# Optimization experiments

Hardware: AMD Instinct MI355X
Metric: run time of the kernel (lower is better)

The kernel has to match this reference:

```python
import jax, jax.numpy as jnp
import numpy as np

B, S, E, H, DK, DV, V, FH = 2, 1024, 1024, 16, 64, 64, 32000, 512


def _posenc(seq_len, d_model, n=10000.0):
    pos = jnp.arange(seq_len, dtype=jnp.float32)[:, None]            # [S,1]
    i2 = jnp.arange(0, d_model, 2, dtype=jnp.float32)                 # [E/2]
    ang = pos / jnp.power(n, i2 / d_model)                            # [S,E/2]
    return jnp.stack([jnp.sin(ang), jnp.cos(ang)], axis=-1).reshape(seq_len, d_model)


def _norm(x, g, b, eps=1e-15):
    m = jnp.mean(x, axis=-1, keepdims=True)
    v = jnp.var(x, axis=-1, keepdims=True)  # unbiased=False
    return g * (x - m) * jax.lax.rsqrt(v + eps) + b


def _ff(x, w1, b1, w2, b2):
    return jax.nn.relu(x @ w1 + b1) @ w2 + b2


def _mha(xq, xkv, wqkv, bqkv, wo, bo, causal):
    # wqkv: [3,H,E,d], bqkv: [3,H,d]  (stacked per-head linears)
    q = jnp.einsum('bse,hek->bhsk', xq, wqkv[0]) + bqkv[0][None, :, None, :]
    k = jnp.einsum('bse,hek->bhsk', xkv, wqkv[1]) + bqkv[1][None, :, None, :]
    v = jnp.einsum('bse,hev->bhsv', xkv, wqkv[2]) + bqkv[2][None, :, None, :]
    s = jnp.einsum('bhqk,bhsk->bhqs', q, k) / jnp.sqrt(jnp.float32(DK))
    if causal:
        mask = jnp.triu(jnp.ones((S, S), dtype=bool), 1)
        s = jnp.where(mask[None, None], -jnp.inf, s)
    p = jax.nn.softmax(s, axis=-1)
    o = jnp.einsum('bhqs,bhsv->bhqv', p, v)
    o = o.transpose(0, 2, 1, 3).reshape(xq.shape[0], S, H * DV)
    return o @ wo + bo


def setup_inputs():
    key = jax.random.key(0)
    ks = iter(jax.random.split(key, 40))

    def rn(shape, scale=0.02):
        return jax.random.normal(next(ks), shape, dtype=jnp.float32) * scale

    inp = {
        'src': jax.random.randint(next(ks), (B, S), 0, V, dtype=jnp.int32),
        'trg': jax.random.randint(next(ks), (B, S), 0, V, dtype=jnp.int32),
        'emb_enc': rn((V, E), 1.0),
        'emb_dec': rn((V, E), 1.0),
        'qkv_e': rn((3, H, E, DK)), 'bqkv_e': rn((3, H, DK)),
        'wo_e': rn((H * DV, E)), 'bo_e': rn((E,)),
        'qkv_m': rn((3, H, E, DK)), 'bqkv_m': rn((3, H, DK)),
        'wo_m': rn((H * DV, E)), 'bo_m': rn((E,)),
        'qkv_c': rn((3, H, E, DK)), 'bqkv_c': rn((3, H, DK)),
        'wo_c': rn((H * DV, E)), 'bo_c': rn((E,)),
        'gamma': jnp.ones((5, E), jnp.float32),
        'beta': jnp.zeros((5, E), jnp.float32),
        'ff_w1': rn((2, E, FH)), 'ff_b1': rn((2, FH)),
        'ff_w2': rn((2, FH, E)), 'ff_b2': rn((2, E)),
        'w_out': rn((E, V)), 'b_out': rn((V,)),
    }
    return inp


def reference(src, trg, emb_enc, emb_dec, qkv_e, bqkv_e, wo_e, bo_e,
              qkv_m, bqkv_m, wo_m, bo_m, qkv_c, bqkv_c, wo_c, bo_c,
              gamma, beta, ff_w1, ff_b1, ff_w2, ff_b2, w_out, b_out):
    pe = _posenc(S, E)
    # ---- encoder ----
    x = emb_enc[src] + pe
    a = _mha(x, x, qkv_e, bqkv_e, wo_e, bo_e, causal=False)
    n1 = _norm(x + a, gamma[0], beta[0])
    f = _ff(n1, ff_w1[0], ff_b1[0], ff_w2[0], ff_b2[0])
    enc = _norm(n1 + f, gamma[1], beta[1])
    # ---- decoder ----
    y = emb_dec[trg] + pe
    a = _mha(y, y, qkv_m, bqkv_m, wo_m, bo_m, causal=True)
    n1d = _norm(y + a, gamma[2], beta[2])
    a2 = _mha(n1d, enc, qkv_c, bqkv_c, wo_c, bo_c, causal=False)
    n2d = _norm(n1d + a2, gamma[3], beta[3])
    f = _ff(n2d, ff_w1[1], ff_b1[1], ff_w2[1], ff_b2[1])
    n3d = _norm(n2d + f, gamma[4], beta[4])
    logits = n3d @ w_out + b_out
    return jax.nn.softmax(logits, axis=-1)
```

## Files before the change

kernel.cpp:

```cpp
#include <hip/hip_runtime.h>
#include <hip/hip_bf16.h>
#include <hip/hip_fp16.h>
#include <math.h>

namespace {

constexpr int kB = 2, kS = 1024, kE = 1024, kH = 16, kD = 64, kV = 32000, kFH = 512;
constexpr int kBS = kB * kS;
constexpr int kHD = kH * kD;

typedef __attribute__((ext_vector_type(8))) short bf16x8;
typedef __attribute__((ext_vector_type(8))) unsigned short u16x8;
typedef __attribute__((ext_vector_type(4))) float f32x4;

#define GLDS(g, l) __builtin_amdgcn_global_load_lds(                          \
      (const __attribute__((address_space(1))) void*)(g),                     \
      (__attribute__((address_space(3))) void*)(l), 16, 0, 0)

struct TSeg {
  const float* src;
  __hip_bfloat16* dst;
  int R, C, bpi, off;
};
struct TcastArgs { TSeg s[11]; };

__global__ __launch_bounds__(256) void prep_k(
    const int* __restrict__ src, const int* __restrict__ trg,
    const float* __restrict__ emb_e, const float* __restrict__ emb_d,
    float* __restrict__ enc_x, __hip_bfloat16* __restrict__ enc_xb,
    float* __restrict__ dec_x, __hip_bfloat16* __restrict__ dec_xb,
    TcastArgs a) {
  int bid = blockIdx.x;
  if (bid < 2 * kBS) {
    int which = bid >> 11;
    int row = bid & (kBS - 1);
    const int* tok = which ? trg : src;
    const float* emb = which ? emb_d : emb_e;
    float* out = which ? dec_x : enc_x;
    __hip_bfloat16* outb = which ? dec_xb : enc_xb;
    int s = row & (kS - 1);
    int t = tok[row];
    const float4* sv4 = (const float4*)(emb + (size_t)t * kE);
    int e4 = threadIdx.x;
    float4 aa = sv4[e4];
    const float kLn = 0.017988946039015984f;
    int p0 = e4 * 2, p1 = p0 + 1;
    float a0 = (float)s * __expf(-(float)p0 * kLn);
    float a1 = (float)s * __expf(-(float)p1 * kLn);
    float4 v = make_float4(aa.x + sinf(a0), aa.y + cosf(a0),
                           aa.z + sinf(a1), aa.w + cosf(a1));
    ((float4*)(out + (size_t)row * kE))[e4] = v;
    union { __hip_bfloat16 h[4]; short4 s4; } u;
    u.h[0] = __float2bfloat16(v.x); u.h[1] = __float2bfloat16(v.y);
    u.h[2] = __float2bfloat16(v.z); u.h[3] = __float2bfloat16(v.w);
    ((short4*)(outb + (size_t)row * kE))[e4] = u.s4;
    return;
  }
  bid -= 2 * kBS;
  __shared__ float tile[32][33];
  int si = 0;
#pragma unroll
  for (int i = 1; i < 11; ++i) si = (bid >= a.s[i].off) ? i : si;
  const TSeg sg = a.s[si];
  int local = bid - sg.off;
  int item = local / sg.bpi;
  int rem  = local % sg.bpi;
  int nbx = sg.C >> 5;
  int c0 = (rem % nbx) * 32, r0 = (rem / nbx) * 32;
  const float* srcp = sg.src + (size_t)item * sg.R * sg.C;
  __hip_bfloat16* dstp = sg.dst + (size_t)item * sg.R * sg.C;
  int tx = threadIdx.x & 31, ty = threadIdx.x >> 5;
#pragma unroll
  for (int i = 0; i < 32; i += 8)
    tile[ty + i][tx] = srcp[(size_t)(r0 + ty + i) * sg.C + c0 + tx];
  __syncthreads();
#pragma unroll
  for (int i = 0; i < 32; i += 8)
    dstp[(size_t)(c0 + ty + i) * sg.R + r0 + tx] = __float2bfloat16(tile[tx][ty + i]);
}

__global__ __launch_bounds__(256) void vtrans_k(const __hip_bfloat16* __restrict__ v,
                                                int sV, __hip_bfloat16* __restrict__ vt) {
  __shared__ unsigned short tile[32][34];
  int s0 = blockIdx.x * 32, d0 = blockIdx.y * 32, bh = blockIdx.z;
  int b = bh >> 4, h = bh & 15;
  int tx = threadIdx.x & 31, ty = threadIdx.x >> 5;
  const unsigned short* src = (const unsigned short*)v;
  unsigned short* dst = (unsigned short*)vt;
#pragma unroll
  for (int i = 0; i < 32; i += 8)
    tile[ty + i][tx] = src[(size_t)(b * kS + s0 + ty + i) * sV + h * 64 + d0 + tx];
  __syncthreads();
#pragma unroll
  for (int i = 0; i < 32; i += 8)
    dst[(size_t)(bh * 64 + d0 + ty + i) * kS + s0 + tx] = tile[tx][ty + i];
}

__global__ __launch_bounds__(256) void gemm_bf16_k(
    const __hip_bfloat16* __restrict__ A,
    const __hip_bfloat16* __restrict__ Bt,
    const float* __restrict__ bias,
    void* __restrict__ Cout,
    int N, int K, int mode, int gridM) {
  __shared__ __align__(16) char L[3][16384];
  const int nwg = gridDim.x, id = blockIdx.x;
  const int swz = (id & 7) * (nwg >> 3) + (id >> 3);
  const int bm = (swz % gridM) * 128, bn = (swz / gridM) * 128;
  const int tid = threadIdx.x, w = tid >> 6, lane = tid & 63;
  const int wr = w >> 1, wc = w & 1;
  const int lr = lane & 15, kg = lane >> 4;
  const int NT = K >> 5;
  const __hip_bfloat16* Ag = A + (size_t)bm * K;
  const __hip_bfloat16* Bg = Bt + (size_t)bn * K;

  auto stage = [&](int t) {
    const int buf = t % 3, k0 = t * 32;
#pragma unroll
    for (int j = 0; j < 2; ++j) {
      int slot = w * 64 + lane + j * 256;
      int row = slot >> 2;
      int cs = (slot & 3) ^ ((row >> 1) & 3);
      GLDS(Ag + (size_t)row * K + k0 + cs * 8, L[buf] + w * 1024 + j * 4096);
      GLDS(Bg + (size_t)row * K + k0 + cs * 8, L[buf] + 8192 + w * 1024 + j * 4096);
    }
  };

  f32x4 acc[4][4] = {};
  stage(0);
  stage(1);
  asm volatile("s_waitcnt vmcnt(4)" ::: "memory");
  __builtin_amdgcn_s_barrier();

  for (int t = 0; t < NT; ++t) {
    const char* buf = L[t % 3];
    if (t + 2 < NT) stage(t + 2);
    bf16x8 af[4], bfr[4];
#pragma unroll
    for (int i = 0; i < 4; ++i) {
      int row = wr * 64 + i * 16 + lr;
      af[i] = *(const bf16x8*)(buf + row * 64 + ((kg ^ ((row >> 1) & 3)) << 4));
    }
#pragma unroll
    for (int j = 0; j < 4; ++j) {
      int row = wc * 64 + j * 16 + lr;
      bfr[j] = *(const bf16x8*)(buf + 8192 + row * 64 + ((kg ^ ((row >> 1) & 3)) << 4));
    }
    __builtin_amdgcn_s_setprio(1);
#pragma unroll
    for (int i = 0; i < 4; ++i)
#pragma unroll
      for (int j = 0; j < 4; ++j)
        acc[i][j] = __builtin_amdgcn_mfma_f32_16x16x32_bf16(af[i], bfr[j], acc[i][j], 0, 0, 0);
    __builtin_amdgcn_s_setprio(0);
    if (t + 2 < NT)
      asm volatile("s_waitcnt vmcnt(4) lgkmcnt(0)" ::: "memory");
    else
      asm volatile("s_waitcnt vmcnt(0) lgkmcnt(0)" ::: "memory");
    __builtin_amdgcn_s_barrier();
  }

  float* Cf = (float*)Cout;
  __hip_bfloat16* Cb = (__hip_bfloat16*)Cout;
#pragma unroll
  for (int j = 0; j < 4; ++j) {
    int col = bn + wc * 64 + j * 16 + lr;
    float bc = bias[col];
#pragma unroll
    for (int i = 0; i < 4; ++i) {
      int rbase = bm + wr * 64 + i * 16 + kg * 4;
#pragma unroll
      for (int r = 0; r < 4; ++r) {
        float val = acc[i][j][r] + bc;
        if (mode & 1) val = fmaxf(val, 0.0f);
        if (mode < 2) Cf[(size_t)(rbase + r) * N + col] = val;
        else          Cb[(size_t)(rbase + r) * N + col] = __float2bfloat16(val);
      }
    }
  }
}

__global__ __launch_bounds__(256) void gemm64_k(
    const __hip_bfloat16* __restrict__ A,
    const __hip_bfloat16* __restrict__ Bt,
    const float* __restrict__ bias,
    void* __restrict__ Cout,
    int N, int K, int mode, int gridM) {
  __shared__ __align__(16) char L[3][8192];
  const int nwg = gridDim.x, id = blockIdx.x;
  const int swz = (id & 7) * (nwg >> 3) + (id >> 3);
  const int bm = (swz % gridM) * 64, bn = (swz / gridM) * 64;
  const int tid = threadIdx.x, w = tid >> 6, lane = tid & 63;
  const int wr = w >> 1, wc = w & 1;
  const int lr = lane & 15, kg = lane >> 4;
  const int NT = K >> 5;
  const __hip_bfloat16* Ag = A + (size_t)bm * K;
  const __hip_bfloat16* Bg = Bt + (size_t)bn * K;

  auto stage = [&](int t) {
    const int buf = t % 3, k0 = t * 32;
    int row = tid >> 2;
    int cs = (tid & 3) ^ ((row >> 1) & 3);
    GLDS(Ag + (size_t)row * K + k0 + cs * 8, L[buf] + tid * 16);
    GLDS(Bg + (size_t)row * K + k0 + cs * 8, L[buf] + 4096 + tid * 16);
  };

  f32x4 acc[2][2] = {};
  stage(0);
  stage(1);
  asm volatile("s_waitcnt vmcnt(2)" ::: "memory");
  __builtin_amdgcn_s_barrier();

  for (int t = 0; t < NT; ++t) {
    const char* buf = L[t % 3];
    if (t + 2 < NT) stage(t + 2);
    bf16x8 af[2], bfr[2];
#pragma unroll
    for (int i = 0; i < 2; ++i) {
      int row = wr * 32 + i * 16 + lr;
      af[i] = *(const bf16x8*)(buf + row * 64 + ((kg ^ ((row >> 1) & 3)) << 4));
    }
#pragma unroll
    for (int j = 0; j < 2; ++j) {
      int row = wc * 32 + j * 16 + lr;
      bfr[j] = *(const bf16x8*)(buf + 4096 + row * 64 + ((kg ^ ((row >> 1) & 3)) << 4));
    }
    __builtin_amdgcn_s_setprio(1);
#pragma unroll
    for (int i = 0; i < 2; ++i)
#pragma unroll
      for (int j = 0; j < 2; ++j)
        acc[i][j] = __builtin_amdgcn_mfma_f32_16x16x32_bf16(af[i], bfr[j], acc[i][j], 0, 0, 0);
    __builtin_amdgcn_s_setprio(0);
    if (t + 2 < NT)
      asm volatile("s_waitcnt vmcnt(2) lgkmcnt(0)" ::: "memory");
    else
      asm volatile("s_waitcnt vmcnt(0) lgkmcnt(0)" ::: "memory");
    __builtin_amdgcn_s_barrier();
  }

  float* Cf = (float*)Cout;
  __hip_bfloat16* Cb = (__hip_bfloat16*)Cout;
#pragma unroll
  for (int j = 0; j < 2; ++j) {
    int col = bn + wc * 32 + j * 16 + lr;
    float bc = bias[col];
#pragma unroll
    for (int i = 0; i < 2; ++i) {
      int rbase = bm + wr * 32 + i * 16 + kg * 4;
#pragma unroll
      for (int r = 0; r < 4; ++r) {
        float val = acc[i][j][r] + bc;
        if (mode & 1) val = fmaxf(val, 0.0f);
        if (mode < 2) Cf[(size_t)(rbase + r) * N + col] = val;
        else          Cb[(size_t)(rbase + r) * N + col] = __float2bfloat16(val);
      }
    }
  }
}

__global__ __launch_bounds__(512, 2) void gemm256_k(
    const __hip_bfloat16* __restrict__ A,
    const __hip_bfloat16* __restrict__ Bt,
    const float* __restrict__ bias,
    __half* __restrict__ C,
    int N, int K, int gridM) {
  __shared__ __align__(16) char L[3][32768];
  const int tid = threadIdx.x, w = tid >> 6, lane = tid & 63;
  const int wm = w >> 2, wn = w & 3;
  const int lr = lane & 15, kg = lane >> 4;
  const int nwg = gridDim.x, id = blockIdx.x;
  const int swz = (id & 7) * (nwg >> 3) + (id >> 3);
  const int bm = (swz % gridM) * 256, bn = (swz / gridM) * 256;
  const int NT = K >> 5;
  const __hip_bfloat16* Ag = A + (size_t)bm * K;
  const __hip_bfloat16* Bg = Bt + (size_t)bn * K;

  auto stage = [&](int t) {
    const int buf = t % 3, k0 = t * 32;
#pragma unroll
    for (int j = 0; j < 2; ++j) {
      int slot = w * 64 + lane + j * 512;
      int row = slot >> 2;
      int cs = (slot & 3) ^ ((row >> 1) & 3);
      GLDS(Ag + (size_t)row * K + k0 + cs * 8, L[buf] + w * 1024 + j * 8192);
      GLDS(Bg + (size_t)row * K + k0 + cs * 8, L[buf] + 16384 + w * 1024 + j * 8192);
    }
  };

  f32x4 acc[8][4] = {};
  stage(0);
  stage(1);
  asm volatile("s_waitcnt vmcnt(4)" ::: "memory");
  __builtin_amdgcn_s_barrier();

  for (int t = 0; t < NT; ++t) {
    const char* buf = L[t % 3];
    if (t + 2 < NT) stage(t + 2);
    bf16x8 af[8], bfr[4];
#pragma unroll
    for (int mg = 0; mg < 8; ++mg) {
      int row = wm * 128 + mg * 16 + lr;
      af[mg] = *(const bf16x8*)(buf + row * 64 + ((kg ^ ((row >> 1) & 3)) << 4));
    }
#pragma unroll
    for (int n = 0; n < 4; ++n) {
      int row = wn * 64 + n * 16 + lr;
      bfr[n] = *(const bf16x8*)(buf + 16384 + row * 64 + ((kg ^ ((row >> 1) & 3)) << 4));
    }
    __builtin_amdgcn_s_setprio(1);
#pragma unroll
    for (int mg = 0; mg < 8; ++mg)
#pragma unroll
      for (int n = 0; n < 4; ++n)
        acc[mg][n] = __builtin_amdgcn_mfma_f32_16x16x32_bf16(af[mg], bfr[n], acc[mg][n], 0, 0, 0);
    __builtin_amdgcn_s_setprio(0);
    if (t + 2 < NT)
      asm volatile("s_waitcnt vmcnt(4) lgkmcnt(0)" ::: "memory");
    else
      asm volatile("s_waitcnt vmcnt(0) lgkmcnt(0)" ::: "memory");
    __builtin_amdgcn_s_barrier();
  }

#pragma unroll
  for (int mg = 0; mg < 8; ++mg) {
    int rbase = bm + wm * 128 + mg * 16 + (kg << 2);
#pragma unroll
    for (int n = 0; n < 4; ++n) {
      int col = bn + (wn << 6) + n * 16 + lr;
      float bc = bias[col];
#pragma unroll
      for (int r = 0; r < 4; ++r)
        C[(size_t)(rbase + r) * N + col] = __float2half(acc[mg][n][r] + bc);
    }
  }
}

__global__ __launch_bounds__(256) void attn_mfma_k(
    const __hip_bfloat16* __restrict__ q, int sQ,
    const __hip_bfloat16* __restrict__ k, int sK,
    const __hip_bfloat16* __restrict__ vt,
    __hip_bfloat16* __restrict__ o,
    int causal) {
  __shared__ __align__(16) char Ks[3][8192];
  __shared__ __align__(16) char Vs[3][8192];
  __shared__ __align__(16) char Ps[4][2304];
  const int tid = threadIdx.x, w = tid >> 6, l = tid & 63;
  const int lr = l & 15, lg = l >> 4;
  const int q0 = blockIdx.x * 64, h = blockIdx.y, b = blockIdx.z;

  const int qrow = q0 + w * 16 + lr;
  const __hip_bfloat16* qp = q + (size_t)(b * kS + qrow) * sQ + h * 64 + lg * 8;
  bf16x8 aQ0 = *(const bf16x8*)qp;
  bf16x8 aQ1 = *(const bf16x8*)(qp + 32);

  f32x4 oacc[4] = {};
  float mrun[4], lrun[4];
#pragma unroll
  for (int r = 0; r < 4; ++r) { mrun[r] = -INFINITY; lrun[r] = 0.0f; }

  const int ntiles = causal ? ((q0 >> 6) + 1) : (kS >> 6);
  const int diagT = causal ? (q0 >> 6) : -1;
  const char* kbase = (const char*)(k + (size_t)(b * kS) * sK + h * 64);
  const char* vbase = (const char*)(vt + (size_t)((b * kH + h) * 64) * kS);
  char* Pw = Ps[w];

  auto stage = [&](int t) {
    const int buf = t % 3, kv0 = t * 64;
#pragma unroll
    for (int i = 0; i < 2; ++i) {
      int slot = w * 128 + i * 64 + l;
      int row = slot >> 3, sl = slot & 7, c = sl ^ (row & 7);
      GLDS(kbase + (size_t)(kv0 + row) * sK * 2 + c * 16, Ks[buf] + (w * 128 + i * 64) * 16);
      GLDS(vbase + (size_t)row * kS * 2 + kv0 * 2 + c * 16, Vs[buf] + (w * 128 + i * 64) * 16);
    }
  };

  stage(0);
  if (ntiles > 1) {
    stage(1);
    asm volatile("s_waitcnt vmcnt(4)" ::: "memory");
  } else {
    asm volatile("s_waitcnt vmcnt(0)" ::: "memory");
  }
  __builtin_amdgcn_s_barrier();

  for (int t = 0; t < ntiles; ++t) {
    const int kv0 = t * 64;
    const char* Kb = Ks[t % 3];
    const char* Vb = Vs[t % 3];
    if (t + 2 < ntiles) stage(t + 2);

    f32x4 sacc[4] = {};
#pragma unroll
    for (int nf = 0; nf < 4; ++nf) {
      int key = nf * 16 + lr;
#pragma unroll
      for (int kf = 0; kf < 2; ++kf) {
        int ch = (lg + kf * 4) ^ (key & 7);
        bf16x8 bK = *(const bf16x8*)(Kb + key * 128 + ch * 16);
        sacc[nf] = __builtin_amdgcn_mfma_f32_16x16x32_bf16(kf ? aQ1 : aQ0, bK, sacc[nf], 0, 0, 0);
      }
    }

#pragma unroll
    for (int r = 0; r < 4; ++r) {
      int row16 = lg * 4 + r;
      int qg = q0 + w * 16 + row16;
      float sv[4];
#pragma unroll
      for (int nf = 0; nf < 4; ++nf) {
        float s = sacc[nf][r] * 0.125f;
        if (t == diagT && (kv0 + nf * 16 + lr) > qg) s = -INFINITY;
        sv[nf] = s;
      }
      float mx = fmaxf(fmaxf(sv[0], sv[1]), fmaxf(sv[2], sv[3]));
#pragma unroll
      for (int m = 1; m < 16; m <<= 1) mx = fmaxf(mx, __shfl_xor(mx, m));
      if (mx > mrun[r] + 8.0f) {
        float sc = __expf(mrun[r] - mx);
        mrun[r] = mx;
        lrun[r] *= sc;
#pragma unroll
        for (int nfd = 0; nfd < 4; ++nfd) oacc[nfd][r] *= sc;
      }
      float base = mrun[r];
      float rs = 0.0f;
#pragma unroll
      for (int nf = 0; nf < 4; ++nf) {
        float p = __expf(sv[nf] - base);
        rs += p;
        *(__hip_bfloat16*)(Pw + row16 * 144 + (nf * 16 + lr) * 2) = __float2bfloat16(p);
      }
#pragma unroll
      for (int m = 1; m < 16; m <<= 1) rs += __shfl_xor(rs, m);
      lrun[r] += rs;
    }

    bf16x8 aP0 = *(const bf16x8*)(Pw + lr * 144 + (lg * 8) * 2);
    bf16x8 aP1 = *(const bf16x8*)(Pw + lr * 144 + (lg * 8 + 32) * 2);
#pragma unroll
    for (int nfd = 0; nfd < 4; ++nfd) {
      int d = nfd * 16 + lr;
#pragma unroll
      for (int kf = 0; kf < 2; ++kf) {
        int ch = (lg + kf * 4) ^ (d & 7);
        bf16x8 bV = *(const bf16x8*)(Vb + d * 128 + ch * 16);
        oacc[nfd] = __builtin_amdgcn_mfma_f32_16x16x32_bf16(kf ? aP1 : aP0, bV, oacc[nfd], 0, 0, 0);
      }
    }

    if (t + 1 < ntiles) {
      if (t + 2 < ntiles)
        asm volatile("s_waitcnt vmcnt(4) lgkmcnt(0)" ::: "memory");
      else
        asm volatile("s_waitcnt vmcnt(0) lgkmcnt(0)" ::: "memory");
      __builtin_amdgcn_s_barrier();
    }
  }

#pragma unroll
  for (int r = 0; r < 4; ++r) {
    float inv = 1.0f / lrun[r];
    int rowg = q0 + w * 16 + lg * 4 + r;
#pragma unroll
    for (int nfd = 0; nfd < 4; ++nfd)
      o[(size_t)(b * kS + rowg) * kHD + h * 64 + nfd * 16 + lr] =
          __float2bfloat16(oacc[nfd][r] * inv);
  }
}

__global__ __launch_bounds__(256) void ln_res_k(const float* __restrict__ a,
                                                const float* __restrict__ b,
                                                const float* __restrict__ gamma,
                                                const float* __restrict__ beta,
                                                float* __restrict__ out,
                                                __hip_bfloat16* __restrict__ outb) {
  __shared__ float sh[10];
  int row = blockIdx.x, tid = threadIdx.x;
  const float4* a4 = (const float4*)(a + (size_t)row * kE);
  const float4* b4 = (const float4*)(b + (size_t)row * kE);
  float4 t = a4[tid], u = b4[tid];
  t.x += u.x; t.y += u.y; t.z += u.z; t.w += u.w;
  float s = t.x + t.y + t.z + t.w;
  float q2 = t.x * t.x + t.y * t.y + t.z * t.z + t.w * t.w;
  for (int o = 32; o > 0; o >>= 1) { s += __shfl_down(s, o); q2 += __shfl_down(q2, o); }
  int lane = tid & 63, wid = tid >> 6;
  if (lane == 0) { sh[wid] = s; sh[4 + wid] = q2; }
  __syncthreads();
  if (tid == 0) {
    float S2 = sh[0] + sh[1] + sh[2] + sh[3];
    float Q2 = sh[4] + sh[5] + sh[6] + sh[7];
    float mean = S2 * (1.0f / kE);
    float var = Q2 * (1.0f / kE) - mean * mean;
    sh[8] = mean;
    sh[9] = rsqrtf(var + 1e-15f);
  }
  __syncthreads();
  float mean = sh[8], inv = sh[9];
  float4 g = ((const float4*)gamma)[tid], be = ((const float4*)beta)[tid];
  float4 v;
  v.x = g.x * ((t.x - mean) * inv) + be.x;
  v.y = g.y * ((t.y - mean) * inv) + be.y;
  v.z = g.z * ((t.z - mean) * inv) + be.z;
  v.w = g.w * ((t.w - mean) * inv) + be.w;
  ((float4*)(out + (size_t)row * kE))[tid] = v;
  union { __hip_bfloat16 h[4]; short4 s4; } uo;
  uo.h[0] = __float2bfloat16(v.x); uo.h[1] = __float2bfloat16(v.y);
  uo.h[2] = __float2bfloat16(v.z); uo.h[3] = __float2bfloat16(v.w);
  ((short4*)(outb + (size_t)row * kE))[tid] = uo.s4;
}

__global__ __launch_bounds__(512) void softmax_rows_k(const __half* __restrict__ lgt,
                                                      float* __restrict__ out) {
  __shared__ float sh[18];
  int row = blockIdx.x;
  const u16x8* x8 = (const u16x8*)(lgt + (size_t)row * kV);
  const int n8 = kV / 8;
  int tid = threadIdx.x;
  u16x8 v[8];
  float m = -INFINITY, sum = 0.0f;
#pragma unroll
  for (int i = 0; i < 8; ++i) {
    int idx = tid + i * 512;
    if (idx < n8) {
      v[i] = x8[idx];
      union { u16x8 u; __half h[8]; } cv; cv.u = v[i];
      float f[8];
#pragma unroll
      for (int j = 0; j < 8; ++j) f[j] = __half2float(cv.h[j]);
      float mx = f[0];
#pragma unroll
      for (int j = 1; j < 8; ++j) mx = fmaxf(mx, f[j]);
      float nm = fmaxf(m, mx);
      float add = 0.0f;
#pragma unroll
      for (int j = 0; j < 8; ++j) add += __expf(f[j] - nm);
      sum = sum * __expf(m - nm) + add;
      m = nm;
    }
  }
  for (int o = 32; o > 0; o >>= 1) {
    float om = __shfl_down(m, o), os = __shfl_down(sum, o);
    float nm = fmaxf(m, om);
    sum = sum * __expf(m - nm) + os * __expf(om - nm);
    m = nm;
  }
  int lane = tid & 63, wid = tid >> 6;
  if (lane == 0) { sh[wid] = m; sh[8 + wid] = sum; }
  __syncthreads();
  if (tid == 0) {
    float M = sh[0], S2 = 0.0f;
#pragma unroll
    for (int i2 = 1; i2 < 8; ++i2) M = fmaxf(M, sh[i2]);
#pragma unroll
    for (int i2 = 0; i2 < 8; ++i2) S2 += sh[8 + i2] * __expf(sh[i2] - M);
    sh[16] = M;
    sh[17] = 1.0f / S2;
  }
  __syncthreads();
  float M = sh[16], rcp = sh[17];
#pragma unroll
  for (int i = 0; i < 8; ++i) {
    int idx = tid + i * 512;
    if (idx < n8) {
      union { u16x8 u; __half h[8]; } cv; cv.u = v[i];
      float4 o0, o1;
      o0.x = __expf(__half2float(cv.h[0]) - M) * rcp;
      o0.y = __expf(__half2float(cv.h[1]) - M) * rcp;
      o0.z = __expf(__half2float(cv.h[2]) - M) * rcp;
      o0.w = __expf(__half2float(cv.h[3]) - M) * rcp;
      o1.x = __expf(__half2float(cv.h[4]) - M) * rcp;
      o1.y = __expf(__half2float(cv.h[5]) - M) * rcp;
      o1.z = __expf(__half2float(cv.h[6]) - M) * rcp;
      o1.w = __expf(__half2float(cv.h[7]) - M) * rcp;
      float* dst = out + (size_t)row * kV + idx * 8;
      ((float4*)dst)[0] = o0;
      ((float4*)dst)[1] = o1;
    }
  }
}

}

extern "C" void kernel_launch(void* const* d_in, const int* in_sizes, int n_in,
                              void* d_out, int out_size, void* d_ws, size_t ws_size,
                              hipStream_t stream) {
  const int*   src    = (const int*)d_in[0];
  const int*   trg    = (const int*)d_in[1];
  const float* emb_e  = (const float*)d_in[2];
  const float* emb_d  = (const float*)d_in[3];
  const float* qkv_e  = (const float*)d_in[4];
  const float* bqkv_e = (const float*)d_in[5];
  const float* wo_e   = (const float*)d_in[6];
  const float* bo_e   = (const float*)d_in[7];
  const float* qkv_m  = (const float*)d_in[8];
  const float* bqkv_m = (const float*)d_in[9];
  const float* wo_m   = (const float*)d_in[10];
  const float* bo_m   = (const float*)d_in[11];
  const float* qkv_c  = (const float*)d_in[12];
  const float* bqkv_c = (const float*)d_in[13];
  const float* wo_c   = (const float*)d_in[14];
  const float* bo_c   = (const float*)d_in[15];
  const float* gamma  = (const float*)d_in[16];
  const float* beta   = (const float*)d_in[17];
  const float* ffw1   = (const float*)d_in[18];
  const float* ffb1   = (const float*)d_in[19];
  const float* ffw2   = (const float*)d_in[20];
  const float* ffb2   = (const float*)d_in[21];
  const float* wout   = (const float*)d_in[22];
  const float* bout   = (const float*)d_in[23];
  float* out = (float*)d_out;

  char* base = (char*)d_ws;
  const size_t R = (size_t)kBS * kE;
  const size_t WE = (size_t)kHD * kE;
  float* enc_x = (float*)base;
  float* dec_x = enc_x + R;
  float* t1    = dec_x + R;
  float* n1    = t1 + R;
  float* n_enc = n1 + R;
  __hip_bfloat16* bb     = (__hip_bfloat16*)(n_enc + R);
  __hip_bfloat16* enc_xb = bb;
  __hip_bfloat16* n1b    = enc_xb + R;
  __hip_bfloat16* n_encb = n1b + R;
  __hip_bfloat16* qkvb   = n_encb + R;
  __hip_bfloat16* kvb    = qkvb + 3 * R;
  __hip_bfloat16* qb1    = kvb + 2 * R;
  __hip_bfloat16* vtb    = qb1 + R;
  __hip_bfloat16* ao16   = vtb + R;
  __hip_bfloat16* ffhb   = ao16 + R;
  __hip_bfloat16* Wqkv_e = ffhb + R / 2;
  __hip_bfloat16* Wqkv_m = Wqkv_e + 3 * WE;
  __hip_bfloat16* Wqkv_c = Wqkv_m + 3 * WE;
  __hip_bfloat16* Wo_e   = Wqkv_c + 3 * WE;
  __hip_bfloat16* Wo_m   = Wo_e + WE;
  __hip_bfloat16* Wo_c   = Wo_m + WE;
  __hip_bfloat16* Wf1a   = Wo_c + WE;
  __hip_bfloat16* Wf1b   = Wf1a + (size_t)kE * kFH;
  __hip_bfloat16* Wf2a   = Wf1b + (size_t)kE * kFH;
  __hip_bfloat16* Wf2b   = Wf2a + (size_t)kFH * kE;
  const size_t lgtBytes = (size_t)kBS * kV * sizeof(__half);
  __hip_bfloat16* dec_xb = (__hip_bfloat16*)(base + lgtBytes);
  __hip_bfloat16* Wv     = dec_xb + R;
  __half* lgt = (__half*)base;

  auto gemmb = [&](const __hip_bfloat16* A, const __hip_bfloat16* Bt, const float* bias,
                   void* C, int M, int N, int K, int mode) {
    int gridM = M / 128;
    gemm_bf16_k<<<dim3(gridM * (N / 128)), 256, 0, stream>>>(A, Bt, bias, C, N, K, mode, gridM);
  };
  auto gemmb64 = [&](const __hip_bfloat16* A, const __hip_bfloat16* Bt, const float* bias,
                     void* C, int M, int N, int K, int mode) {
    int gridM = M / 64;
    gemm64_k<<<dim3(gridM * (N / 64)), 256, 0, stream>>>(A, Bt, bias, C, N, K, mode, gridM);
  };
  auto vtrans = [&](const __hip_bfloat16* v, int sV) {
    vtrans_k<<<dim3(kS / 32, kD / 32, kB * kH), 256, 0, stream>>>(v, sV, vtb);
  };
  auto attn = [&](const __hip_bfloat16* q, int sQ, const __hip_bfloat16* k, int sK,
                  int causal) {
    attn_mfma_k<<<dim3(kS / 64, kH, kB), 256, 0, stream>>>(q, sQ, k, sK, vtb, ao16, causal);
  };
  auto ln = [&](const float* a, const float* b2, int sel, float* o1, __hip_bfloat16* o2) {
    ln_res_k<<<kBS, 256, 0, stream>>>(a, b2, gamma + sel * kE, beta + sel * kE, o1, o2);
  };

  {
    TcastArgs a;
    const size_t EF = (size_t)kE * kFH;
    a.s[0]  = {qkv_e,       Wqkv_e, kE, kD,   64,    0};
    a.s[1]  = {qkv_m,       Wqkv_m, kE, kD,   64,    3072};
    a.s[2]  = {qkv_c,       Wqkv_c, kE, kD,   64,    6144};
    a.s[3]  = {wo_e,        Wo_e,   kHD, kE,  1024,  9216};
    a.s[4]  = {wo_m,        Wo_m,   kHD, kE,  1024,  10240};
    a.s[5]  = {wo_c,        Wo_c,   kHD, kE,  1024,  11264};
    a.s[6]  = {ffw1,        Wf1a,   kE, kFH,  512,   12288};
    a.s[7]  = {ffw1 + EF,   Wf1b,   kE, kFH,  512,   12800};
    a.s[8]  = {ffw2,        Wf2a,   kFH, kE,  512,   13312};
    a.s[9]  = {ffw2 + EF,   Wf2b,   kFH, kE,  512,   13824};
    a.s[10] = {wout,        Wv,     kE, kV,   32000, 14336};
    prep_k<<<2 * kBS + 46336, 256, 0, stream>>>(src, trg, emb_e, emb_d,
                                                enc_x, enc_xb, dec_x, dec_xb, a);
  }

  gemmb(enc_xb, Wqkv_e, bqkv_e, qkvb, kBS, 3 * kHD, kE, 2);
  vtrans(qkvb + 2 * kHD, 3 * kHD);
  attn(qkvb, 3 * kHD, qkvb + kHD, 3 * kHD, 0);
  gemmb64(ao16, Wo_e, bo_e, t1, kBS, kE, kHD, 0);
  ln(enc_x, t1, 0, n1, n1b);
  gemmb64(n1b, Wf1a, ffb1, ffhb, kBS, kFH, kE, 3);
  gemmb64(ffhb, Wf2a, ffb2, t1, kBS, kE, kFH, 0);
  ln(n1, t1, 1, n_enc, n_encb);

  gemmb(dec_xb, Wqkv_m, bqkv_m, qkvb, kBS, 3 * kHD, kE, 2);
  vtrans(qkvb + 2 * kHD, 3 * kHD);
  attn(qkvb, 3 * kHD, qkvb + kHD, 3 * kHD, 1);
  gemmb64(ao16, Wo_m, bo_m, t1, kBS, kE, kHD, 0);
  ln(dec_x, t1, 2, n1, n1b);

  gemmb64(n1b, Wqkv_c, bqkv_c, qb1, kBS, kHD, kE, 2);
  gemmb64(n_encb, Wqkv_c + WE, bqkv_c + kHD, kvb, kBS, 2 * kHD, kE, 2);
  vtrans(kvb + kHD, 2 * kHD);
  attn(qb1, kHD, kvb, 2 * kHD, 0);
  gemmb64(ao16, Wo_c, bo_c, t1, kBS, kE, kHD, 0);
  ln(n1, t1, 3, enc_x, enc_xb);

  gemmb64(enc_xb, Wf1b, ffb1 + kFH, ffhb, kBS, kFH, kE, 3);
  gemmb64(ffhb, Wf2b, ffb2 + kE, t1, kBS, kE, kFH, 0);
  ln(enc_x, t1, 4, dec_x, dec_xb);

  gemm256_k<<<dim3((kBS / 256) * (kV / 256)), 512, 0, stream>>>(
      dec_xb, Wv, bout, lgt, kV, kE, kBS / 256);
  softmax_rows_k<<<kBS, 512, 0, stream>>>(lgt, out);
}
```

Before: 611.7 us.

## Batch independent encoder and decoder self-attention stages into dual-launch kernels

Encoder and decoder self-attention chains are independent, so the QKV GEMM, V transpose, attention, output projection and layernorm for both now run as single launches that pick their operands from the grid index. This doubles the work per launch, aiming to fill the GPU better and cut launch overhead and tail effects. The workspace is re-laid out at fixed MiB offsets with aliased buffers, and the unused fp32 layernorm outputs are skipped. The aliasing carries a risk of overlapping live buffers.

```diff
diff --git a/kernel.cpp b/kernel.cpp
--- a/kernel.cpp
+++ b/kernel.cpp
@@ -8,6 +8,7 @@
 constexpr int kB = 2, kS = 1024, kE = 1024, kH = 16, kD = 64, kV = 32000, kFH = 512;
 constexpr int kBS = kB * kS;
 constexpr int kHD = kH * kD;
+constexpr size_t kMiB = 1u << 20;
 
 typedef __attribute__((ext_vector_type(8))) short bf16x8;
 typedef __attribute__((ext_vector_type(8))) unsigned short u16x8;
@@ -79,10 +80,9 @@
     dstp[(size_t)(c0 + ty + i) * sg.R + r0 + tx] = __float2bfloat16(tile[tx][ty + i]);
 }
 
-__global__ __launch_bounds__(256) void vtrans_k(const __hip_bfloat16* __restrict__ v,
-                                                int sV, __hip_bfloat16* __restrict__ vt) {
+__device__ __forceinline__ void vtrans_body(const __hip_bfloat16* v, int sV,
+                                            __hip_bfloat16* vt, int s0, int d0, int bh) {
   __shared__ unsigned short tile[32][34];
-  int s0 = blockIdx.x * 32, d0 = blockIdx.y * 32, bh = blockIdx.z;
   int b = bh >> 4, h = bh & 15;
   int tx = threadIdx.x & 31, ty = threadIdx.x >> 5;
   const unsigned short* src = (const unsigned short*)v;
@@ -96,14 +96,24 @@
     dst[(size_t)(bh * 64 + d0 + ty + i) * kS + s0 + tx] = tile[tx][ty + i];
 }
 
-__global__ __launch_bounds__(256) void gemm_bf16_k(
-    const __hip_bfloat16* __restrict__ A,
-    const __hip_bfloat16* __restrict__ Bt,
-    const float* __restrict__ bias,
-    void* __restrict__ Cout,
-    int N, int K, int mode, int gridM) {
+__global__ __launch_bounds__(256) void vtrans_k(const __hip_bfloat16* __restrict__ v,
+                                                int sV, __hip_bfloat16* __restrict__ vt) {
+  vtrans_body(v, sV, vt, blockIdx.x * 32, blockIdx.y * 32, blockIdx.z);
+}
+
+__global__ __launch_bounds__(256) void vtrans_dual_k(
+    const __hip_bfloat16* __restrict__ v0, __hip_bfloat16* __restrict__ vt0,
+    const __hip_bfloat16* __restrict__ v1, __hip_bfloat16* __restrict__ vt1, int sV) {
+  int z = blockIdx.z;
+  int which = z >> 5, bh = z & 31;
+  vtrans_body(which ? v1 : v0, sV, which ? vt1 : vt0,
+              blockIdx.x * 32, blockIdx.y * 32, bh);
+}
+
+__device__ __forceinline__ void gemm128_body(
+    const __hip_bfloat16* A, const __hip_bfloat16* Bt, const float* bias, void* Cout,
+    int N, int K, int mode, int gridM, int id, int nwg) {
   __shared__ __align__(16) char L[3][16384];
-  const int nwg = gridDim.x, id = blockIdx.x;
   const int swz = (id & 7) * (nwg >> 3) + (id >> 3);
   const int bm = (swz % gridM) * 128, bn = (swz / gridM) * 128;
   const int tid = threadIdx.x, w = tid >> 6, lane = tid & 63;
@@ -179,14 +189,25 @@
   }
 }
 
-__global__ __launch_bounds__(256) void gemm64_k(
-    const __hip_bfloat16* __restrict__ A,
-    const __hip_bfloat16* __restrict__ Bt,
-    const float* __restrict__ bias,
-    void* __restrict__ Cout,
+struct G2 { const __hip_bfloat16* A; const __hip_bfloat16* Bt; const float* bias; void* C; };
+
+__global__ __launch_bounds__(256) void gemm_bf16_k(
+    const __hip_bfloat16* __restrict__ A, const __hip_bfloat16* __restrict__ Bt,
+    const float* __restrict__ bias, void* __restrict__ Cout,
     int N, int K, int mode, int gridM) {
+  gemm128_body(A, Bt, bias, Cout, N, K, mode, gridM, blockIdx.x, gridDim.x);
+}
+
+__global__ __launch_bounds__(256) void gemm_dual_k(G2 g0, G2 g1, int N, int K,
+                                                   int mode, int gridM) {
+  const G2& g = blockIdx.y ? g1 : g0;
+  gemm128_body(g.A, g.Bt, g.bias, g.C, N, K, mode, gridM, blockIdx.x, gridDim.x);
+}
+
+__device__ __forceinline__ void gemm64_body(
+    const __hip_bfloat16* A, const __hip_bfloat16* Bt, const float* bias, void* Cout,
+    int N, int K, int mode, int gridM, int id, int nwg) {
   __shared__ __align__(16) char L[3][8192];
-  const int nwg = gridDim.x, id = blockIdx.x;
   const int swz = (id & 7) * (nwg >> 3) + (id >> 3);
   const int bm = (swz % gridM) * 64, bn = (swz / gridM) * 64;
   const int tid = threadIdx.x, w = tid >> 6, lane = tid & 63;
@@ -258,11 +279,22 @@
   }
 }
 
+__global__ __launch_bounds__(256) void gemm64_k(
+    const __hip_bfloat16* __restrict__ A, const __hip_bfloat16* __restrict__ Bt,
+    const float* __restrict__ bias, void* __restrict__ Cout,
+    int N, int K, int mode, int gridM) {
+  gemm64_body(A, Bt, bias, Cout, N, K, mode, gridM, blockIdx.x, gridDim.x);
+}
+
+__global__ __launch_bounds__(256) void gemm64_dual_k(G2 g0, G2 g1, int N, int K,
+                                                     int mode, int gridM) {
+  const G2& g = blockIdx.y ? g1 : g0;
+  gemm64_body(g.A, g.Bt, g.bias, g.C, N, K, mode, gridM, blockIdx.x, gridDim.x);
+}
+
 __global__ __launch_bounds__(512, 2) void gemm256_k(
-    const __hip_bfloat16* __restrict__ A,
-    const __hip_bfloat16* __restrict__ Bt,
-    const float* __restrict__ bias,
-    __half* __restrict__ C,
+    const __hip_bfloat16* __restrict__ A, const __hip_bfloat16* __restrict__ Bt,
+    const float* __restrict__ bias, __half* __restrict__ C,
     int N, int K, int gridM) {
   __shared__ __align__(16) char L[3][32768];
   const int tid = threadIdx.x, w = tid >> 6, lane = tid & 63;
@@ -335,18 +367,15 @@
   }
 }
 
-__global__ __launch_bounds__(256) void attn_mfma_k(
-    const __hip_bfloat16* __restrict__ q, int sQ,
-    const __hip_bfloat16* __restrict__ k, int sK,
-    const __hip_bfloat16* __restrict__ vt,
-    __hip_bfloat16* __restrict__ o,
-    int causal) {
+__device__ __forceinline__ void attn_body(
+    const __hip_bfloat16* q, int sQ, const __hip_bfloat16* k, int sK,
+    const __hip_bfloat16* vt, __hip_bfloat16* o, int causal, int qblk, int h, int b) {
   __shared__ __align__(16) char Ks[3][8192];
   __shared__ __align__(16) char Vs[3][8192];
   __shared__ __align__(16) char Ps[4][2304];
   const int tid = threadIdx.x, w = tid >> 6, l = tid & 63;
   const int lr = l & 15, lg = l >> 4;
-  const int q0 = blockIdx.x * 64, h = blockIdx.y, b = blockIdx.z;
+  const int q0 = qblk * 64;
 
   const int qrow = q0 + w * 16 + lr;
   const __hip_bfloat16* qp = q + (size_t)(b * kS + qrow) * sQ + h * 64 + lg * 8;
@@ -358,8 +387,8 @@
 #pragma unroll
   for (int r = 0; r < 4; ++r) { mrun[r] = -INFINITY; lrun[r] = 0.0f; }
 
-  const int ntiles = causal ? ((q0 >> 6) + 1) : (kS >> 6);
-  const int diagT = causal ? (q0 >> 6) : -1;
+  const int ntiles = causal ? (qblk + 1) : (kS >> 6);
+  const int diagT = causal ? qblk : -1;
   const char* kbase = (const char*)(k + (size_t)(b * kS) * sK + h * 64);
   const char* vbase = (const char*)(vt + (size_t)((b * kH + h) * 64) * kS);
   char* Pw = Ps[w];
@@ -469,14 +498,29 @@
   }
 }
 
-__global__ __launch_bounds__(256) void ln_res_k(const float* __restrict__ a,
-                                                const float* __restrict__ b,
-                                                const float* __restrict__ gamma,
-                                                const float* __restrict__ beta,
-                                                float* __restrict__ out,
-                                                __hip_bfloat16* __restrict__ outb) {
+__global__ __launch_bounds__(256) void attn_mfma_k(
+    const __hip_bfloat16* __restrict__ q, int sQ,
+    const __hip_bfloat16* __restrict__ k, int sK,
+    const __hip_bfloat16* __restrict__ vt,
+    __hip_bfloat16* __restrict__ o, int causal) {
+  attn_body(q, sQ, k, sK, vt, o, causal, blockIdx.x, blockIdx.y, blockIdx.z);
+}
+
+struct A2 { const __hip_bfloat16* q; const __hip_bfloat16* k;
+            const __hip_bfloat16* vt; __hip_bfloat16* o; int causal; };
+
+__global__ __launch_bounds__(256) void attn_dual_k(A2 a0, A2 a1, int sQ, int sK) {
+  int z = blockIdx.z;
+  int which = z >> 1, b = z & 1;
+  const A2& a = which ? a1 : a0;
+  attn_body(a.q, sQ, a.k, sK, a.vt, a.o, a.causal, blockIdx.x, blockIdx.y, b);
+}
+
+__device__ __forceinline__ void ln_body(const float* a, const float* b,
+                                        const float* gamma, const float* beta,
+                                        float* out, __hip_bfloat16* outb, int row) {
   __shared__ float sh[10];
-  int row = blockIdx.x, tid = threadIdx.x;
+  int tid = threadIdx.x;
   const float4* a4 = (const float4*)(a + (size_t)row * kE);
   const float4* b4 = (const float4*)(b + (size_t)row * kE);
   float4 t = a4[tid], u = b4[tid];
@@ -503,11 +547,30 @@
   v.y = g.y * ((t.y - mean) * inv) + be.y;
   v.z = g.z * ((t.z - mean) * inv) + be.z;
   v.w = g.w * ((t.w - mean) * inv) + be.w;
-  ((float4*)(out + (size_t)row * kE))[tid] = v;
+  if (out) ((float4*)(out + (size_t)row * kE))[tid] = v;
   union { __hip_bfloat16 h[4]; short4 s4; } uo;
   uo.h[0] = __float2bfloat16(v.x); uo.h[1] = __float2bfloat16(v.y);
   uo.h[2] = __float2bfloat16(v.z); uo.h[3] = __float2bfloat16(v.w);
   ((short4*)(outb + (size_t)row * kE))[tid] = uo.s4;
+}
+
+__global__ __launch_bounds__(256) void ln_res_k(const float* __restrict__ a,
+                                                const float* __restrict__ b,
+                                                const float* __restrict__ gamma,
+                                                const float* __restrict__ beta,
+                                                float* __restrict__ out,
+                                                __hip_bfloat16* __restrict__ outb) {
+  ln_body(a, b, gamma, beta, out, outb, blockIdx.x);
+}
+
+struct L2 { const float* a; const float* b; const float* gamma; const float* beta;
+            float* out; __hip_bfloat16* outb; };
+
+__global__ __launch_bounds__(256) void ln_dual_k(L2 l0, L2 l1) {
+  int which = blockIdx.x >> 11;
+  int row = blockIdx.x & (kBS - 1);
+  const L2& l = which ? l1 : l0;
+  ln_body(l.a, l.b, l.gamma, l.beta, l.out, l.outb, row);
 }
 
 __global__ __launch_bounds__(512) void softmax_rows_k(const __half* __restrict__ lgt,
@@ -614,52 +677,44 @@
   char* base = (char*)d_ws;
   const size_t R = (size_t)kBS * kE;
   const size_t WE = (size_t)kHD * kE;
-  float* enc_x = (float*)base;
-  float* dec_x = enc_x + R;
-  float* t1    = dec_x + R;
-  float* n1    = t1 + R;
-  float* n_enc = n1 + R;
-  __hip_bfloat16* bb     = (__hip_bfloat16*)(n_enc + R);
-  __hip_bfloat16* enc_xb = bb;
-  __hip_bfloat16* n1b    = enc_xb + R;
-  __hip_bfloat16* n_encb = n1b + R;
-  __hip_bfloat16* qkvb   = n_encb + R;
-  __hip_bfloat16* kvb    = qkvb + 3 * R;
-  __hip_bfloat16* qb1    = kvb + 2 * R;
-  __hip_bfloat16* vtb    = qb1 + R;
-  __hip_bfloat16* ao16   = vtb + R;
-  __hip_bfloat16* ffhb   = ao16 + R;
-  __hip_bfloat16* Wqkv_e = ffhb + R / 2;
-  __hip_bfloat16* Wqkv_m = Wqkv_e + 3 * WE;
-  __hip_bfloat16* Wqkv_c = Wqkv_m + 3 * WE;
-  __hip_bfloat16* Wo_e   = Wqkv_c + 3 * WE;
-  __hip_bfloat16* Wo_m   = Wo_e + WE;
-  __hip_bfloat16* Wo_c   = Wo_m + WE;
-  __hip_bfloat16* Wf1a   = Wo_c + WE;
-  __hip_bfloat16* Wf1b   = Wf1a + (size_t)kE * kFH;
-  __hip_bfloat16* Wf2a   = Wf1b + (size_t)kE * kFH;
-  __hip_bfloat16* Wf2b   = Wf2a + (size_t)kFH * kE;
+  float* enc_x = (float*)(base + 0 * kMiB);
+  float* dec_x = (float*)(base + 8 * kMiB);
+  float* n1e   = (float*)(base + 16 * kMiB);
+  float* n1d   = (float*)(base + 24 * kMiB);
+  __hip_bfloat16* enc_xb = (__hip_bfloat16*)(base + 32 * kMiB);
+  __hip_bfloat16* n1e_b  = (__hip_bfloat16*)(base + 36 * kMiB);
+  __hip_bfloat16* n1d_b  = (__hip_bfloat16*)(base + 40 * kMiB);
+  __hip_bfloat16* n_encb = (__hip_bfloat16*)(base + 44 * kMiB);
+  __hip_bfloat16* qkvb_e = (__hip_bfloat16*)(base + 48 * kMiB);
+  __hip_bfloat16* qkvb_m = (__hip_bfloat16*)(base + 60 * kMiB);
+  float* t1e = (float*)(base + 48 * kMiB);
+  float* t1m = (float*)(base + 56 * kMiB);
+  __hip_bfloat16* kvb = (__hip_bfloat16*)(base + 64 * kMiB);
+  __hip_bfloat16* vt_e = (__hip_bfloat16*)(base + 72 * kMiB);
+  __hip_bfloat16* vt_m = (__hip_bfloat16*)(base + 76 * kMiB);
+  __hip_bfloat16* ffhb = (__hip_bfloat16*)(base + 76 * kMiB);
+  __hip_bfloat16* ao_e = (__hip_bfloat16*)(base + 80 * kMiB);
+  __hip_bfloat16* ao_m = (__hip_bfloat16*)(base + 84 * kMiB);
+  __hip_bfloat16* qb1  = (__hip_bfloat16*)(base + 84 * kMiB);
+  __hip_bfloat16* Wqkv_e = (__hip_bfloat16*)(base + 88 * kMiB);
+  __hip_bfloat16* Wqkv_m = (__hip_bfloat16*)(base + 94 * kMiB);
+  __hip_bfloat16* Wqkv_c = (__hip_bfloat16*)(base + 100 * kMiB);
+  __hip_bfloat16* Wo_e   = (__hip_bfloat16*)(base + 106 * kMiB);
+  __hip_bfloat16* Wo_m   = (__hip_bfloat16*)(base + 108 * kMiB);
+  __hip_bfloat16* Wo_c   = (__hip_bfloat16*)(base + 110 * kMiB);
+  __hip_bfloat16* Wf1a   = (__hip_bfloat16*)(base + 112 * kMiB);
+  __hip_bfloat16* Wf1b   = (__hip_bfloat16*)(base + 113 * kMiB);
+  __hip_bfloat16* Wf2a   = (__hip_bfloat16*)(base + 114 * kMiB);
+  __hip_bfloat16* Wf2b   = (__hip_bfloat16*)(base + 115 * kMiB);
   const size_t lgtBytes = (size_t)kBS * kV * sizeof(__half);
   __hip_bfloat16* dec_xb = (__hip_bfloat16*)(base + lgtBytes);
   __hip_bfloat16* Wv     = dec_xb + R;
   __half* lgt = (__half*)base;
 
-  auto gemmb = [&](const __hip_bfloat16* A, const __hip_bfloat16* Bt, const float* bias,
-                   void* C, int M, int N, int K, int mode) {
-    int gridM = M / 128;
-    gemm_bf16_k<<<dim3(gridM * (N / 128)), 256, 0, stream>>>(A, Bt, bias, C, N, K, mode, gridM);
-  };
-  auto gemmb64 = [&](const __hip_bfloat16* A, const __hip_bfloat16* Bt, const float* bias,
+  auto gemm64s = [&](const __hip_bfloat16* A, const __hip_bfloat16* Bt, const float* bias,
                      void* C, int M, int N, int K, int mode) {
     int gridM = M / 64;
     gemm64_k<<<dim3(gridM * (N / 64)), 256, 0, stream>>>(A, Bt, bias, C, N, K, mode, gridM);
-  };
-  auto vtrans = [&](const __hip_bfloat16* v, int sV) {
-    vtrans_k<<<dim3(kS / 32, kD / 32, kB * kH), 256, 0, stream>>>(v, sV, vtb);
-  };
-  auto attn = [&](const __hip_bfloat16* q, int sQ, const __hip_bfloat16* k, int sK,
-                  int causal) {
-    attn_mfma_k<<<dim3(kS / 64, kH, kB), 256, 0, stream>>>(q, sQ, k, sK, vtb, ao16, causal);
   };
   auto ln = [&](const float* a, const float* b2, int sel, float* o1, __hip_bfloat16* o2) {
     ln_res_k<<<kBS, 256, 0, stream>>>(a, b2, gamma + sel * kE, beta + sel * kE, o1, o2);
@@ -683,31 +738,34 @@
                                                 enc_x, enc_xb, dec_x, dec_xb, a);
   }
 
-  gemmb(enc_xb, Wqkv_e, bqkv_e, qkvb, kBS, 3 * kHD, kE, 2);
-  vtrans(qkvb + 2 * kHD, 3 * kHD);
-  attn(qkvb, 3 * kHD, qkvb + kHD, 3 * kHD, 0);
-  gemmb64(ao16, Wo_e, bo_e, t1, kBS, kE, kHD, 0);
-  ln(enc_x, t1, 0, n1, n1b);
-  gemmb64(n1b, Wf1a, ffb1, ffhb, kBS, kFH, kE, 3);
-  gemmb64(ffhb, Wf2a, ffb2, t1, kBS, kE, kFH, 0);
-  ln(n1, t1, 1, n_enc, n_encb);
-
-  gemmb(dec_xb, Wqkv_m, bqkv_m, qkvb, kBS, 3 * kHD, kE, 2);
-  vtrans(qkvb + 2 * kHD, 3 * kHD);
-  attn(qkvb, 3 * kHD, qkvb + kHD, 3 * kHD, 1);
-  gemmb64(ao16, Wo_m, bo_m, t1, kBS, kE, kHD, 0);
-  ln(dec_x, t1, 2, n1, n1b);
-
-  gemmb64(n1b, Wqkv_c, bqkv_c, qb1, kBS, kHD, kE, 2);
-  gemmb64(n_encb, Wqkv_c + WE, bqkv_c + kHD, kvb, kBS, 2 * kHD, kE, 2);
-  vtrans(kvb + kHD, 2 * kHD);
-  attn(qb1, kHD, kvb, 2 * kHD, 0);
-  gemmb64(ao16, Wo_c, bo_c, t1, kBS, kE, kHD, 0);
-  ln(n1, t1, 3, enc_x, enc_xb);
-
-  gemmb64(enc_xb, Wf1b, ffb1 + kFH, ffhb, kBS, kFH, kE, 3);
-  gemmb64(ffhb, Wf2b, ffb2 + kE, t1, kBS, kE, kFH, 0);
-  ln(enc_x, t1, 4, dec_x, dec_xb);
+  gemm_dual_k<<<dim3(16 * 24, 2), 256, 0, stream>>>(
+      G2{enc_xb, Wqkv_e, bqkv_e, qkvb_e}, G2{dec_xb, Wqkv_m, bqkv_m, qkvb_m},
+      3 * kHD, kE, 2, 16);
+  vtrans_dual_k<<<dim3(kS / 32, kD / 32, 2 * kB * kH), 256, 0, stream>>>(
+      qkvb_e + 2 * kHD, vt_e, qkvb_m + 2 * kHD, vt_m, 3 * kHD);
+  attn_dual_k<<<dim3(kS / 64, kH, 2 * kB), 256, 0, stream>>>(
+      A2{qkvb_e, qkvb_e + kHD, vt_e, ao_e, 0},
+      A2{qkvb_m, qkvb_m + kHD, vt_m, ao_m, 1}, 3 * kHD, 3 * kHD);
+  gemm64_dual_k<<<dim3(32 * 16, 2), 256, 0, stream>>>(
+      G2{ao_e, Wo_e, bo_e, t1e}, G2{ao_m, Wo_m, bo_m, t1m}, kE, kHD, 0, 32);
+  ln_dual_k<<<2 * kBS, 256, 0, stream>>>(
+      L2{enc_x, t1e, gamma + 0 * kE, beta + 0 * kE, n1e, n1e_b},
+      L2{dec_x, t1m, gamma + 2 * kE, beta + 2 * kE, n1d, n1d_b});
+
+  gemm64s(n1e_b, Wf1a, ffb1, ffhb, kBS, kFH, kE, 3);
+  gemm64s(n1d_b, Wqkv_c, bqkv_c, qb1, kBS, kHD, kE, 2);
+  gemm64s(ffhb, Wf2a, ffb2, t1e, kBS, kE, kFH, 0);
+  ln(n1e, t1e, 1, nullptr, n_encb);
+
+  gemm64s(n_encb, Wqkv_c + WE, bqkv_c + kHD, kvb, kBS, 2 * kHD, kE, 2);
+  vtrans_k<<<dim3(kS / 32, kD / 32, kB * kH), 256, 0, stream>>>(kvb + kHD, 2 * kHD, vt_e);
+  attn_mfma_k<<<dim3(kS / 64, kH, kB), 256, 0, stream>>>(qb1, kHD, kvb, 2 * kHD, vt_e, ao_e, 0);
+  gemm64s(ao_e, Wo_c, bo_c, t1m, kBS, kE, kHD, 0);
+  ln(n1d, t1m, 3, enc_x, enc_xb);
+
+  gemm64s(enc_xb, Wf1b, ffb1 + kFH, ffhb, kBS, kFH, kE, 3);
+  gemm64s(ffhb, Wf2b, ffb2 + kE, t1e, kBS, kE, kFH, 0);
+  ln(enc_x, t1e, 4, nullptr, dec_xb);
 
   gemm256_k<<<dim3((kBS / 256) * (kV / 256)), 512, 0, stream>>>(
       dec_xb, Wv, bout, lgt, kV, kE, kBS / 256);
```

New measurement: 592.4 us. 1.03x faster.
